# Kernel optimization log

Hardware: AMD Instinct MI355X
Metric: run time of the kernel (lower is better)

## Reference

```python
import jax, jax.numpy as jnp
import numpy as np

B, S, H = 128, 256, 768


def setup_inputs() -> dict:
    key = jax.random.key(0)
    ks = jax.random.split(key, 8)
    sc = 0.02
    return {
        "p": jax.random.normal(ks[0], (B, S, H), dtype=jnp.float32),
        "option_len": jax.random.randint(ks[1], (B,), 0, S - 1, dtype=jnp.int32),
        # SingleMatchNet params
        "Wt": jax.random.normal(ks[2], (H, H), dtype=jnp.float32) * sc,
        "bt": jnp.zeros((H,), dtype=jnp.float32),
        "Wd": jax.random.normal(ks[3], (H, H), dtype=jnp.float32) * sc,
        "bd": jnp.zeros((H,), dtype=jnp.float32),
        # AOI.dense3
        "Wd3": jax.random.normal(ks[4], (H, 3 * H), dtype=jnp.float32) * sc,
        "bd3": jnp.zeros((H,), dtype=jnp.float32),
        # FuseNet params
        "W1": jax.random.normal(ks[5], (H, H), dtype=jnp.float32) * sc,
        "b1": jnp.zeros((H,), dtype=jnp.float32),
        "W2": jax.random.normal(ks[6], (H, H), dtype=jnp.float32) * sc,
        "b2": jnp.zeros((H,), dtype=jnp.float32),
    }


def reference(p, option_len, Wt, bt, Wd, bd, Wd3, bd3, W1, b1, W2, b2):
    b, s, h = p.shape
    # For each option i, the 3 other options of its 4-option group, ascending
    others_tab = jnp.array([[1, 2, 3], [0, 2, 3], [0, 1, 3], [0, 1, 2]])
    idx = jnp.arange(b)
    others = (idx // 4)[:, None] * 4 + others_tab[idx % 4]  # [B,3]

    q = p[others]                         # [B,3,S,H] comparison options
    lens = option_len[others] + 1         # [B,3] key lengths (as in torch code)

    trans_q = q @ Wt.T + bt               # [B,3,S,H]
    att = jnp.einsum('bsh,bkth->bkst', p, trans_q)  # [B,3,S,S]

    # masked_softmax: softmax(scores*mask), zero masked, renormalize (+1e-13)
    mask = (jnp.arange(s)[None, None, None, :] < lens[:, :, None, None]).astype(p.dtype)
    sm = jax.nn.softmax(att * mask, axis=-1) * mask
    sm = sm / (sm.sum(axis=-1, keepdims=True) + 1e-13)

    att_vec = jnp.einsum('bkst,bkth->bksh', sm, q)      # [B,3,S,H]
    oc_k = jax.nn.relu(att_vec @ Wd.T + bd)             # [B,3,S,H]

    # cat along feature dim in k-order (oc1,oc2,oc3) -> [B,S,3H]
    cat_oc = oc_k.transpose(0, 2, 1, 3).reshape(b, s, 3 * h)
    oc = cat_oc @ Wd3.T + bd3                           # [B,S,H]

    # FuseNet([op, oc]): mid = sigmoid(linear1(oc) + linear2(op))
    mid = jax.nn.sigmoid(oc @ W1.T + b1 + p @ W2.T + b2)
    return p * mid + oc * (1 - mid)
```

## Files before the change

### kernel.cpp

```cpp
#include <hip/hip_runtime.h>
#include <hip/hip_bf16.h>

constexpr int Sq = 256;
constexpr int Hq = 768;
constexpr int EW = Hq * Hq;

typedef __attribute__((ext_vector_type(4))) float f32x4;
typedef __attribute__((ext_vector_type(8))) short bf16x8;

__device__ __forceinline__ float bf2f(unsigned short u) {
  unsigned int x = ((unsigned int)u) << 16;
  float f;
  __builtin_memcpy(&f, &x, 4);
  return f;
}
__device__ __forceinline__ unsigned short f2bf(float f) {
  unsigned int x;
  __builtin_memcpy(&x, &f, 4);
  unsigned int lsb = (x >> 16) & 1u;
  x += 0x7fffu + lsb;
  return (unsigned short)(x >> 16);
}
__device__ __forceinline__ ushort4 cvt4(float4 v) {
  ushort4 o;
  o.x = f2bf(v.x);
  o.y = f2bf(v.y);
  o.z = f2bf(v.z);
  o.w = f2bf(v.w);
  return o;
}
__device__ __forceinline__ void cvt4split(float4 v, ushort4& h, ushort4& l) {
  h.x = f2bf(v.x);
  l.x = f2bf(v.x - bf2f(h.x));
  h.y = f2bf(v.y);
  l.y = f2bf(v.y - bf2f(h.y));
  h.z = f2bf(v.z);
  l.z = f2bf(v.z - bf2f(h.z));
  h.w = f2bf(v.w);
  l.w = f2bf(v.w - bf2f(h.w));
}

__device__ __forceinline__ int other_of(int b, int k) {
  int i = b & 3;
  int jl = k + (k >= i ? 1 : 0);
  return (b & ~3) + jl;
}

constexpr int LDP = 32;

__device__ __forceinline__ int swz8(int row) { return ((row >> 1) & 3) << 3; }

__device__ __forceinline__ void gload16(const unsigned short* g, unsigned short* s) {
  __builtin_amdgcn_global_load_lds((const __attribute__((address_space(1))) unsigned int*)g,
                                   (__attribute__((address_space(3))) unsigned int*)s, 16, 0, 0);
}

template <int ROWS>
__device__ __forceinline__ void dma_b16(const unsigned short* __restrict__ G, int lda, int kk,
                                        unsigned short* __restrict__ S, int tid) {
#pragma unroll
  for (int pp = 0; pp < ROWS / 64; ++pp) {
    int idx = tid + pp * 256;
    int row = idx >> 2;
    int c8 = ((idx & 3) << 3) ^ swz8(row);
    gload16(G + (long)row * lda + kk + c8, S + idx * 8);
  }
}

template <int ROWS>
__device__ __forceinline__ void stage_f32(const float* __restrict__ G, int lda, int kk,
                                          unsigned short* __restrict__ S, int tid) {
#pragma unroll
  for (int pp = 0; pp < ROWS / 32; ++pp) {
    int idx = tid + pp * 256;
    int row = idx >> 3;
    int c4 = (idx & 7) << 2;
    float4 v = *(const float4*)(G + (long)row * lda + kk + c4);
    *(ushort4*)(&S[row * LDP + (c4 ^ swz8(row))]) = cvt4(v);
  }
}

template <int ROWS>
__device__ __forceinline__ void stage_f32_split(const float* __restrict__ G, int lda, int kk,
                                                unsigned short* __restrict__ Sh,
                                                unsigned short* __restrict__ Sl, int tid) {
#pragma unroll
  for (int pp = 0; pp < ROWS / 32; ++pp) {
    int idx = tid + pp * 256;
    int row = idx >> 3;
    int c4 = (idx & 7) << 2;
    float4 v = *(const float4*)(G + (long)row * lda + kk + c4);
    ushort4 h, l;
    cvt4split(v, h, l);
    int cs = c4 ^ swz8(row);
    *(ushort4*)(&Sh[row * LDP + cs]) = h;
    *(ushort4*)(&Sl[row * LDP + cs]) = l;
  }
}

__global__ __launch_bounds__(256) void k_prep_p(const float* __restrict__ p,
                                                unsigned short* __restrict__ ph,
                                                unsigned short* __restrict__ pl) {
  const long n4 = (long)128 * Sq * Hq / 4;
  const long stride = (long)gridDim.x * blockDim.x;
  for (long i = (long)blockIdx.x * blockDim.x + threadIdx.x; i < n4; i += stride) {
    float4 v = ((const float4*)p)[i];
    ushort4 h, l;
    cvt4split(v, h, l);
    ((ushort4*)ph)[i] = h;
    ((ushort4*)pl)[i] = l;
  }
}

__global__ __launch_bounds__(256) void k_prep_w(const float* __restrict__ Wt,
                                                const float* __restrict__ Wd,
                                                const float* __restrict__ Wd3,
                                                const float* __restrict__ W1,
                                                const float* __restrict__ W2,
                                                unsigned short* __restrict__ wb) {
  const int NW4 = EW / 4;
  const int stride = gridDim.x * blockDim.x;
  ushort4* Wth = (ushort4*)(wb);
  ushort4* Wtl = (ushort4*)(wb + EW);
  ushort4* Wdb = (ushort4*)(wb + 2 * EW);
  ushort4* W1b = (ushort4*)(wb + 3 * EW);
  ushort4* W2b = (ushort4*)(wb + 4 * EW);
  ushort4* Wd3b = (ushort4*)(wb + 5 * EW);
  for (int i = blockIdx.x * blockDim.x + threadIdx.x; i < NW4; i += stride) {
    float4 v = ((const float4*)Wt)[i];
    ushort4 h, l;
    cvt4split(v, h, l);
    Wth[i] = h;
    Wtl[i] = l;
    Wdb[i] = cvt4(((const float4*)Wd)[i]);
    W1b[i] = cvt4(((const float4*)W1)[i]);
    W2b[i] = cvt4(((const float4*)W2)[i]);
  }
  for (int i = blockIdx.x * blockDim.x + threadIdx.x; i < 3 * NW4; i += stride)
    Wd3b[i] = cvt4(((const float4*)Wd3)[i]);
}

template <bool A_F32, bool B_F32>
__device__ __forceinline__ void gemm_tile(const void* __restrict__ Av, int lda,
                                          const void* __restrict__ Bv, int ldb, int K,
                                          f32x4 acc[4][4]) {
  __shared__ __align__(16) unsigned short As[128 * LDP];
  __shared__ __align__(16) unsigned short Bs[128 * LDP];
  const int tid = threadIdx.x;
  const int lane = tid & 63;
  const int wid = tid >> 6;
  const int wr = (wid >> 1) << 6;
  const int wc = (wid & 1) << 6;
  const int q4 = lane >> 4;
  const int l16 = lane & 15;

#pragma unroll
  for (int mi = 0; mi < 4; ++mi)
#pragma unroll
    for (int ni = 0; ni < 4; ++ni) acc[mi][ni] = (f32x4){0.f, 0.f, 0.f, 0.f};

  for (int kk = 0; kk < K; kk += 32) {
    __syncthreads();
    if constexpr (A_F32)
      stage_f32<128>((const float*)Av, lda, kk, As, tid);
    else
      dma_b16<128>((const unsigned short*)Av, lda, kk, As, tid);
    if constexpr (B_F32)
      stage_f32<128>((const float*)Bv, ldb, kk, Bs, tid);
    else
      dma_b16<128>((const unsigned short*)Bv, ldb, kk, Bs, tid);
    __syncthreads();
    bf16x8 af[4], bfr[4];
#pragma unroll
    for (int mi = 0; mi < 4; ++mi) {
      int rr = wr + mi * 16 + l16;
      af[mi] = *(const bf16x8*)(&As[rr * LDP + ((q4 << 3) ^ swz8(rr))]);
    }
#pragma unroll
    for (int ni = 0; ni < 4; ++ni) {
      int rr = wc + ni * 16 + l16;
      bfr[ni] = *(const bf16x8*)(&Bs[rr * LDP + ((q4 << 3) ^ swz8(rr))]);
    }
#pragma unroll
    for (int mi = 0; mi < 4; ++mi)
#pragma unroll
      for (int ni = 0; ni < 4; ++ni)
        acc[mi][ni] =
            __builtin_amdgcn_mfma_f32_16x16x32_bf16(af[mi], bfr[ni], acc[mi][ni], 0, 0, 0);
  }
}

__device__ __forceinline__ void gemm_tile_split(const unsigned short* __restrict__ Ahp,
                                                const unsigned short* __restrict__ Alp, int lda,
                                                const float* __restrict__ B, int ldb, int K,
                                                f32x4 acc[4][4]) {
  __shared__ __align__(16) unsigned short Ah[128 * LDP], Al[128 * LDP];
  __shared__ __align__(16) unsigned short Bh[128 * LDP], Bl[128 * LDP];
  const int tid = threadIdx.x;
  const int lane = tid & 63;
  const int wid = tid >> 6;
  const int wr = (wid >> 1) << 6;
  const int wc = (wid & 1) << 6;
  const int q4 = lane >> 4;
  const int l16 = lane & 15;

#pragma unroll
  for (int mi = 0; mi < 4; ++mi)
#pragma unroll
    for (int ni = 0; ni < 4; ++ni) acc[mi][ni] = (f32x4){0.f, 0.f, 0.f, 0.f};

  for (int kk = 0; kk < K; kk += 32) {
    __syncthreads();
    dma_b16<128>(Ahp, lda, kk, Ah, tid);
    dma_b16<128>(Alp, lda, kk, Al, tid);
    stage_f32_split<128>(B, ldb, kk, Bh, Bl, tid);
    __syncthreads();
    bf16x8 ah[4], al[4], bh[4], bl[4];
#pragma unroll
    for (int mi = 0; mi < 4; ++mi) {
      int rr = wr + mi * 16 + l16;
      int co = (q4 << 3) ^ swz8(rr);
      ah[mi] = *(const bf16x8*)(&Ah[rr * LDP + co]);
      al[mi] = *(const bf16x8*)(&Al[rr * LDP + co]);
    }
#pragma unroll
    for (int ni = 0; ni < 4; ++ni) {
      int rr = wc + ni * 16 + l16;
      int co = (q4 << 3) ^ swz8(rr);
      bh[ni] = *(const bf16x8*)(&Bh[rr * LDP + co]);
      bl[ni] = *(const bf16x8*)(&Bl[rr * LDP + co]);
    }
#pragma unroll
    for (int mi = 0; mi < 4; ++mi)
#pragma unroll
      for (int ni = 0; ni < 4; ++ni) {
        acc[mi][ni] =
            __builtin_amdgcn_mfma_f32_16x16x32_bf16(ah[mi], bh[ni], acc[mi][ni], 0, 0, 0);
        acc[mi][ni] =
            __builtin_amdgcn_mfma_f32_16x16x32_bf16(ah[mi], bl[ni], acc[mi][ni], 0, 0, 0);
        acc[mi][ni] =
            __builtin_amdgcn_mfma_f32_16x16x32_bf16(al[mi], bh[ni], acc[mi][ni], 0, 0, 0);
      }
  }
}

__device__ __forceinline__ void gemm_tile_split_b16(const unsigned short* __restrict__ Ahp,
                                                    const unsigned short* __restrict__ Alp, int lda,
                                                    const unsigned short* __restrict__ Bhp,
                                                    const unsigned short* __restrict__ Blp, int ldb,
                                                    int K, f32x4 acc[4][4]) {
  __shared__ __align__(16) unsigned short Ah[128 * LDP], Al[128 * LDP];
  __shared__ __align__(16) unsigned short Bh[128 * LDP], Bl[128 * LDP];
  const int tid = threadIdx.x;
  const int lane = tid & 63;
  const int wid = tid >> 6;
  const int wr = (wid >> 1) << 6;
  const int wc = (wid & 1) << 6;
  const int q4 = lane >> 4;
  const int l16 = lane & 15;

#pragma unroll
  for (int mi = 0; mi < 4; ++mi)
#pragma unroll
    for (int ni = 0; ni < 4; ++ni) acc[mi][ni] = (f32x4){0.f, 0.f, 0.f, 0.f};

  for (int kk = 0; kk < K; kk += 32) {
    __syncthreads();
    dma_b16<128>(Ahp, lda, kk, Ah, tid);
    dma_b16<128>(Alp, lda, kk, Al, tid);
    dma_b16<128>(Bhp, ldb, kk, Bh, tid);
    dma_b16<128>(Blp, ldb, kk, Bl, tid);
    __syncthreads();
    bf16x8 ah[4], al[4], bh[4], bl[4];
#pragma unroll
    for (int mi = 0; mi < 4; ++mi) {
      int rr = wr + mi * 16 + l16;
      int co = (q4 << 3) ^ swz8(rr);
      ah[mi] = *(const bf16x8*)(&Ah[rr * LDP + co]);
      al[mi] = *(const bf16x8*)(&Al[rr * LDP + co]);
    }
#pragma unroll
    for (int ni = 0; ni < 4; ++ni) {
      int rr = wc + ni * 16 + l16;
      int co = (q4 << 3) ^ swz8(rr);
      bh[ni] = *(const bf16x8*)(&Bh[rr * LDP + co]);
      bl[ni] = *(const bf16x8*)(&Bl[rr * LDP + co]);
    }
#pragma unroll
    for (int mi = 0; mi < 4; ++mi)
#pragma unroll
      for (int ni = 0; ni < 4; ++ni) {
        acc[mi][ni] =
            __builtin_amdgcn_mfma_f32_16x16x32_bf16(ah[mi], bh[ni], acc[mi][ni], 0, 0, 0);
        acc[mi][ni] =
            __builtin_amdgcn_mfma_f32_16x16x32_bf16(ah[mi], bl[ni], acc[mi][ni], 0, 0, 0);
        acc[mi][ni] =
            __builtin_amdgcn_mfma_f32_16x16x32_bf16(al[mi], bh[ni], acc[mi][ni], 0, 0, 0);
      }
  }
}

#define EPI_BEGIN()                                        \
  const int lane = threadIdx.x & 63;                       \
  const int wid = threadIdx.x >> 6;                        \
  const int wr = (wid >> 1) << 6, wc = (wid & 1) << 6;     \
  const int q4 = lane >> 4, l16 = lane & 15;               \
  _Pragma("unroll") for (int mi = 0; mi < 4; ++mi)         \
      _Pragma("unroll") for (int ni = 0; ni < 4; ++ni)

template <bool WF32>
__global__ __launch_bounds__(256) void k_tp(const unsigned short* __restrict__ ph,
                                            const unsigned short* __restrict__ pl,
                                            const void* __restrict__ Wh,
                                            const void* __restrict__ Wl,
                                            const float* __restrict__ bt,
                                            unsigned short* __restrict__ tph,
                                            unsigned short* __restrict__ tpl) {
  const int bm = blockIdx.x * 128, bn = blockIdx.y * 128;
  f32x4 acc[4][4];
  if constexpr (WF32)
    gemm_tile_split(ph + (long)bm * Hq, pl + (long)bm * Hq, Hq,
                    (const float*)Wh + (long)bn * Hq, Hq, Hq, acc);
  else
    gemm_tile_split_b16(ph + (long)bm * Hq, pl + (long)bm * Hq, Hq,
                        (const unsigned short*)Wh + (long)bn * Hq,
                        (const unsigned short*)Wl + (long)bn * Hq, Hq, Hq, acc);
  const bool has_lo = (tpl != nullptr);
  EPI_BEGIN() {
    int col = bn + wc + ni * 16 + l16;
    float bv = bt[col];
#pragma unroll
    for (int r = 0; r < 4; ++r) {
      int row = bm + wr + mi * 16 + q4 * 4 + r;
      float v = acc[mi][ni][r] + bv;
      unsigned short h = f2bf(v);
      tph[(long)row * Hq + col] = h;
      if (has_lo) tpl[(long)row * Hq + col] = f2bf(v - bf2f(h));
    }
  }
}

template <bool WF32>
__global__ __launch_bounds__(256) void k_pd(const unsigned short* __restrict__ ph,
                                            const void* __restrict__ Wd,
                                            unsigned short* __restrict__ pdT) {
  const int bm = blockIdx.x * 128, bn = blockIdx.y * 128;
  f32x4 acc[4][4];
  if constexpr (WF32)
    gemm_tile<false, true>(ph + (long)bm * Hq, Hq, (const float*)Wd + (long)bn * Hq, Hq, Hq, acc);
  else
    gemm_tile<false, false>(ph + (long)bm * Hq, Hq, (const unsigned short*)Wd + (long)bn * Hq,
                            Hq, Hq, acc);
  EPI_BEGIN() {
    int col = bn + wc + ni * 16 + l16;
    int rbase = bm + wr + mi * 16 + (q4 << 2);
    int b = rbase >> 8, s0 = rbase & 255;
    ushort4 o;
    o.x = f2bf(acc[mi][ni][0]);
    o.y = f2bf(acc[mi][ni][1]);
    o.z = f2bf(acc[mi][ni][2]);
    o.w = f2bf(acc[mi][ni][3]);
    *(ushort4*)(pdT + ((long)b * Hq + col) * Sq + s0) = o;
  }
}

__global__ __launch_bounds__(256, 1) void k_attsm(const unsigned short* __restrict__ ph,
                                                  const unsigned short* __restrict__ pl,
                                                  const unsigned short* __restrict__ tph,
                                                  const unsigned short* __restrict__ tpl,
                                                  const int* __restrict__ olen,
                                                  unsigned short* __restrict__ sm) {
  const int lin = blockIdx.x + 2 * blockIdx.y;
  const int w = (lin & 7) * 96 + (lin >> 3);
  const int batch = w >> 1;
  const int bm = (w & 1) * 128;

  const int b = batch / 3, k = batch % 3;
  const int j = other_of(b, k);
  const int len = olen[j] + 1;
  const int tid = threadIdx.x;
  const int lane = tid & 63;
  const int wid = tid >> 6;
  const int wr = (wid >> 1) << 6;
  const int wc = (wid & 1) << 7;
  const int half = wid & 1;
  const int q4 = lane >> 4, l16 = lane & 15;
  const bool has_lo = (tpl != nullptr);

  __shared__ __align__(16) unsigned short Ah[128 * LDP], Al[128 * LDP];
  __shared__ __align__(16) unsigned short Bh[256 * LDP], Bl[256 * LDP];
  __shared__ float red[256];

  const unsigned short* Aph = ph + ((long)b * Sq + bm) * Hq;
  const unsigned short* Apl = pl + ((long)b * Sq + bm) * Hq;
  const unsigned short* Bph = tph + (long)j * Sq * Hq;
  const unsigned short* Bpl = has_lo ? tpl + (long)j * Sq * Hq : nullptr;

  f32x4 acc[4][8];
#pragma unroll
  for (int mi = 0; mi < 4; ++mi)
#pragma unroll
    for (int ni = 0; ni < 8; ++ni) acc[mi][ni] = (f32x4){0.f, 0.f, 0.f, 0.f};

  for (int kk = 0; kk < Hq; kk += 32) {
    __syncthreads();
    dma_b16<128>(Aph, Hq, kk, Ah, tid);
    dma_b16<128>(Apl, Hq, kk, Al, tid);
    dma_b16<256>(Bph, Hq, kk, Bh, tid);
    if (has_lo) dma_b16<256>(Bpl, Hq, kk, Bl, tid);
    __syncthreads();
    bf16x8 ah[4], al[4];
#pragma unroll
    for (int mi = 0; mi < 4; ++mi) {
      int rr = wr + mi * 16 + l16;
      int co = (q4 << 3) ^ swz8(rr);
      ah[mi] = *(const bf16x8*)(&Ah[rr * LDP + co]);
      al[mi] = *(const bf16x8*)(&Al[rr * LDP + co]);
    }
#pragma unroll
    for (int ni = 0; ni < 8; ++ni) {
      int rr = wc + ni * 16 + l16;
      int co = (q4 << 3) ^ swz8(rr);
      bf16x8 bh = *(const bf16x8*)(&Bh[rr * LDP + co]);
#pragma unroll
      for (int mi = 0; mi < 4; ++mi) {
        acc[mi][ni] = __builtin_amdgcn_mfma_f32_16x16x32_bf16(ah[mi], bh, acc[mi][ni], 0, 0, 0);
        acc[mi][ni] = __builtin_amdgcn_mfma_f32_16x16x32_bf16(al[mi], bh, acc[mi][ni], 0, 0, 0);
      }
      if (has_lo) {
        bf16x8 bl = *(const bf16x8*)(&Bl[rr * LDP + co]);
#pragma unroll
        for (int mi = 0; mi < 4; ++mi)
          acc[mi][ni] = __builtin_amdgcn_mfma_f32_16x16x32_bf16(ah[mi], bl, acc[mi][ni], 0, 0, 0);
      }
    }
  }

  bool cm[8];
#pragma unroll
  for (int ni = 0; ni < 8; ++ni) cm[ni] = (wc + ni * 16 + l16) >= len;
#pragma unroll
  for (int mi = 0; mi < 4; ++mi)
#pragma unroll
    for (int ni = 0; ni < 8; ++ni)
      if (cm[ni]) acc[mi][ni] = (f32x4){0.f, 0.f, 0.f, 0.f};

  float rmax[4][4];
#pragma unroll
  for (int mi = 0; mi < 4; ++mi)
#pragma unroll
    for (int r = 0; r < 4; ++r) {
      float m = acc[mi][0][r];
#pragma unroll
      for (int ni = 1; ni < 8; ++ni) m = fmaxf(m, acc[mi][ni][r]);
#pragma unroll
      for (int off = 1; off <= 8; off <<= 1) m = fmaxf(m, __shfl_xor(m, off, 64));
      rmax[mi][r] = m;
    }
  if (l16 == 0) {
#pragma unroll
    for (int mi = 0; mi < 4; ++mi)
#pragma unroll
      for (int r = 0; r < 4; ++r) red[(wr + mi * 16 + q4 * 4 + r) * 2 + half] = rmax[mi][r];
  }
  __syncthreads();
#pragma unroll
  for (int mi = 0; mi < 4; ++mi)
#pragma unroll
    for (int r = 0; r < 4; ++r) {
      int row = wr + mi * 16 + q4 * 4 + r;
      rmax[mi][r] = fmaxf(red[row * 2], red[row * 2 + 1]);
    }
  __syncthreads();

  float rsum[4][4];
#pragma unroll
  for (int mi = 0; mi < 4; ++mi)
#pragma unroll
    for (int r = 0; r < 4; ++r) rsum[mi][r] = 0.f;
#pragma unroll
  for (int mi = 0; mi < 4; ++mi)
#pragma unroll
    for (int ni = 0; ni < 8; ++ni)
#pragma unroll
      for (int r = 0; r < 4; ++r) {
        float e = __expf(acc[mi][ni][r] - rmax[mi][r]);
        acc[mi][ni][r] = e;
        if (!cm[ni]) rsum[mi][r] += e;
      }
#pragma unroll
  for (int mi = 0; mi < 4; ++mi)
#pragma unroll
    for (int r = 0; r < 4; ++r) {
#pragma unroll
      for (int off = 1; off <= 8; off <<= 1) rsum[mi][r] += __shfl_xor(rsum[mi][r], off, 64);
    }
  if (l16 == 0) {
#pragma unroll
    for (int mi = 0; mi < 4; ++mi)
#pragma unroll
      for (int r = 0; r < 4; ++r) red[(wr + mi * 16 + q4 * 4 + r) * 2 + half] = rsum[mi][r];
  }
  __syncthreads();

  const float nm = (float)(Sq - len);
  unsigned short* srow = sm + (long)batch * Sq * Sq;
#pragma unroll
  for (int mi = 0; mi < 4; ++mi)
#pragma unroll
    for (int r = 0; r < 4; ++r) {
      int row = wr + mi * 16 + q4 * 4 + r;
      float su = red[row * 2] + red[row * 2 + 1];
      float em = __expf(-rmax[mi][r]);
      float zs = su + nm * em;
      float fs = 1.f / (su + 1e-13f * zs);
      unsigned short* o = srow + (long)(bm + row) * Sq + wc + l16;
#pragma unroll
      for (int ni = 0; ni < 8; ++ni)
        o[ni * 16] = f2bf(cm[ni] ? 0.f : acc[mi][ni][r] * fs);
    }
}

__global__ __launch_bounds__(256) void k_occ(const unsigned short* __restrict__ sm,
                                             const unsigned short* __restrict__ pdT,
                                             const float* __restrict__ bd,
                                             unsigned short* __restrict__ occ) {
  const int lin = blockIdx.x + 2 * (blockIdx.y + 6 * blockIdx.z);
  const int w = (lin & 7) * 576 + (lin >> 3);
  const int t = w >> 1;
  const int bm = (w & 1) * 128, bn = (t % 6) * 128;
  const int batch = t / 6;

  const int b = batch / 3, k = batch % 3;
  const int j = other_of(b, k);
  f32x4 acc[4][4];
  gemm_tile<false, false>(sm + (long)batch * Sq * Sq + (long)bm * Sq, Sq,
                          pdT + ((long)j * Hq + bn) * Sq, Sq, Sq, acc);
  EPI_BEGIN() {
    int col = bn + wc + ni * 16 + l16;
    float bv = bd[col];
#pragma unroll
    for (int r = 0; r < 4; ++r) {
      int s = bm + wr + mi * 16 + q4 * 4 + r;
      occ[((long)(b * Sq + s) * 3 + k) * Hq + col] = f2bf(fmaxf(acc[mi][ni][r] + bv, 0.f));
    }
  }
}

template <bool WF32>
__global__ __launch_bounds__(256) void k_oc(const unsigned short* __restrict__ occ,
                                            const void* __restrict__ Wd3,
                                            const float* __restrict__ bd3,
                                            unsigned short* __restrict__ oc) {
  const int bm = blockIdx.x * 128, bn = blockIdx.y * 128;
  f32x4 acc[4][4];
  if constexpr (WF32)
    gemm_tile<false, true>(occ + (long)bm * 3 * Hq, 3 * Hq,
                           (const float*)Wd3 + (long)bn * 3 * Hq, 3 * Hq, 3 * Hq, acc);
  else
    gemm_tile<false, false>(occ + (long)bm * 3 * Hq, 3 * Hq,
                            (const unsigned short*)Wd3 + (long)bn * 3 * Hq, 3 * Hq, 3 * Hq, acc);
  EPI_BEGIN() {
    int col = bn + wc + ni * 16 + l16;
    float bv = bd3[col];
#pragma unroll
    for (int r = 0; r < 4; ++r) {
      int row = bm + wr + mi * 16 + q4 * 4 + r;
      oc[(long)row * Hq + col] = f2bf(acc[mi][ni][r] + bv);
    }
  }
}

template <bool WF32>
__global__ __launch_bounds__(256) void k_g1(const unsigned short* __restrict__ oc,
                                            const void* __restrict__ W1,
                                            const float* __restrict__ b1,
                                            const float* __restrict__ b2,
                                            unsigned short* __restrict__ g1) {
  const int bm = blockIdx.x * 128, bn = blockIdx.y * 128;
  f32x4 acc[4][4];
  if constexpr (WF32)
    gemm_tile<false, true>(oc + (long)bm * Hq, Hq, (const float*)W1 + (long)bn * Hq, Hq, Hq, acc);
  else
    gemm_tile<false, false>(oc + (long)bm * Hq, Hq, (const unsigned short*)W1 + (long)bn * Hq,
                            Hq, Hq, acc);
  EPI_BEGIN() {
    int col = bn + wc + ni * 16 + l16;
    float bv = b1[col] + b2[col];
#pragma unroll
    for (int r = 0; r < 4; ++r) {
      int row = bm + wr + mi * 16 + q4 * 4 + r;
      g1[(long)row * Hq + col] = f2bf(acc[mi][ni][r] + bv);
    }
  }
}

template <bool WF32>
__global__ __launch_bounds__(256) void k_out(const float* __restrict__ p,
                                             const void* __restrict__ W2,
                                             const unsigned short* __restrict__ g1,
                                             const unsigned short* __restrict__ oc,
                                             float* __restrict__ out) {
  const int bm = blockIdx.x * 128, bn = blockIdx.y * 128;
  f32x4 acc[4][4];
  if constexpr (WF32)
    gemm_tile<true, true>(p + (long)bm * Hq, Hq, (const float*)W2 + (long)bn * Hq, Hq, Hq, acc);
  else
    gemm_tile<true, false>(p + (long)bm * Hq, Hq, (const unsigned short*)W2 + (long)bn * Hq,
                           Hq, Hq, acc);
  EPI_BEGIN() {
    int col = bn + wc + ni * 16 + l16;
#pragma unroll
    for (int r = 0; r < 4; ++r) {
      int row = bm + wr + mi * 16 + q4 * 4 + r;
      long idx = (long)row * Hq + col;
      float g = acc[mi][ni][r] + bf2f(g1[idx]);
      float mid = 1.f / (1.f + __expf(-g));
      float pv = p[idx];
      float ov = bf2f(oc[idx]);
      out[idx] = pv * mid + ov * (1.f - mid);
    }
  }
}

extern "C" void kernel_launch(void* const* d_in, const int* in_sizes, int n_in, void* d_out,
                              int out_size, void* d_ws, size_t ws_size, hipStream_t stream) {
  const float* p = (const float*)d_in[0];
  const int* olen = (const int*)d_in[1];
  const float* Wt = (const float*)d_in[2];
  const float* bt = (const float*)d_in[3];
  const float* Wd = (const float*)d_in[4];
  const float* bd = (const float*)d_in[5];
  const float* Wd3 = (const float*)d_in[6];
  const float* bd3 = (const float*)d_in[7];
  const float* W1 = (const float*)d_in[8];
  const float* b1 = (const float*)d_in[9];
  const float* W2 = (const float*)d_in[10];
  const float* b2 = (const float*)d_in[11];
  float* out = (float*)d_out;

  char* ws = (char*)d_ws;
  const long U = 50331648L;
  const long WB = 9437184L;

  if (ws_size >= (size_t)(WB + 5 * U)) {
    unsigned short* wb = (unsigned short*)(ws);
    unsigned short* ph = (unsigned short*)(ws + WB);
    unsigned short* pl = (unsigned short*)(ws + WB + 1 * U);
    unsigned short* tph = (unsigned short*)(ws + WB + 2 * U);
    unsigned short* tpl = (unsigned short*)(ws + WB + 3 * U);
    unsigned short* sm = (unsigned short*)(ws + WB + 4 * U);
    unsigned short* pdT = (unsigned short*)(ws + WB + 3 * U);
    unsigned short* occ = (unsigned short*)(ws + WB);
    unsigned short* oc = (unsigned short*)(ws + WB + 3 * U);
    unsigned short* g1 = (unsigned short*)(ws + WB + 4 * U);

    k_prep_p<<<2048, 256, 0, stream>>>(p, ph, pl);
    k_prep_w<<<512, 256, 0, stream>>>(Wt, Wd, Wd3, W1, W2, wb);
    k_tp<false><<<dim3(256, 6), 256, 0, stream>>>(ph, pl, wb, wb + EW, bt, tph, tpl);
    k_attsm<<<dim3(2, 384), 256, 0, stream>>>(ph, pl, tph, tpl, olen, sm);
    k_pd<false><<<dim3(256, 6), 256, 0, stream>>>(ph, wb + 2 * EW, pdT);
    k_occ<<<dim3(2, 6, 384), 256, 0, stream>>>(sm, pdT, bd, occ);
    k_oc<false><<<dim3(256, 6), 256, 0, stream>>>(occ, wb + 5 * EW, bd3, oc);
    k_g1<false><<<dim3(256, 6), 256, 0, stream>>>(oc, wb + 3 * EW, b1, b2, g1);
    k_out<false><<<dim3(256, 6), 256, 0, stream>>>(p, wb + 4 * EW, g1, oc, out);
  } else {
    unsigned short* tph = (unsigned short*)(ws + 0 * U);
    unsigned short* tpl = nullptr;
    unsigned short* ph = (unsigned short*)(ws + 1 * U);
    unsigned short* pl = (unsigned short*)(ws + 2 * U);
    unsigned short* occ = (unsigned short*)(ws + 0 * U);
    unsigned short* pdT = (unsigned short*)(ws + 3 * U);
    unsigned short* oc = (unsigned short*)(ws + 3 * U);
    unsigned short* sm = (unsigned short*)(ws + 4 * U);
    unsigned short* g1 = (unsigned short*)(ws + 4 * U);

    k_prep_p<<<2048, 256, 0, stream>>>(p, ph, pl);
    k_tp<true><<<dim3(256, 6), 256, 0, stream>>>(ph, pl, Wt, nullptr, bt, tph, tpl);
    k_pd<true><<<dim3(256, 6), 256, 0, stream>>>(ph, Wd, pdT);
    k_attsm<<<dim3(2, 384), 256, 0, stream>>>(ph, pl, tph, tpl, olen, sm);
    k_occ<<<dim3(2, 6, 384), 256, 0, stream>>>(sm, pdT, bd, occ);
    k_oc<true><<<dim3(256, 6), 256, 0, stream>>>(occ, Wd3, bd3, oc);
    k_g1<true><<<dim3(256, 6), 256, 0, stream>>>(oc, W1, b1, b2, g1);
    k_out<true><<<dim3(256, 6), 256, 0, stream>>>(p, W2, g1, oc, out);
  }
}
```

Baseline: 966.5 us.

## Double-buffer LDS tiles in GEMMs and load attention A operand directly from global

Converts the shared GEMM tile loops and the attention-score kernel to double-buffered LDS staging. The next K-slice is staged while MFMAs run on the current one, which removes one barrier per iteration. In the attention kernel the A operand (p hi/lo) is now read straight from global memory into registers instead of being staged in LDS, and launch bounds are raised to allow two blocks per CU. This roughly doubles B-tile LDS use and adds uncoalesced global A loads in exchange for more overlap and occupancy. An extra barrier is added before the reduction buffer is reused.

New measurement: 938.1 us (median of 2 runs). 1.03x faster.

```diff
diff --git a/kernel.cpp b/kernel.cpp
--- a/kernel.cpp
+++ b/kernel.cpp
@@ -144,8 +144,8 @@
 __device__ __forceinline__ void gemm_tile(const void* __restrict__ Av, int lda,
                                           const void* __restrict__ Bv, int ldb, int K,
                                           f32x4 acc[4][4]) {
-  __shared__ __align__(16) unsigned short As[128 * LDP];
-  __shared__ __align__(16) unsigned short Bs[128 * LDP];
+  __shared__ __align__(16) unsigned short As[2][128 * LDP];
+  __shared__ __align__(16) unsigned short Bs[2][128 * LDP];
   const int tid = threadIdx.x;
   const int lane = tid & 63;
   const int wid = tid >> 6;
@@ -159,34 +159,49 @@
 #pragma unroll
     for (int ni = 0; ni < 4; ++ni) acc[mi][ni] = (f32x4){0.f, 0.f, 0.f, 0.f};
 
-  for (int kk = 0; kk < K; kk += 32) {
-    __syncthreads();
+  auto STAGE = [&](int kk, int bi) {
     if constexpr (A_F32)
-      stage_f32<128>((const float*)Av, lda, kk, As, tid);
+      stage_f32<128>((const float*)Av, lda, kk, As[bi], tid);
     else
-      dma_b16<128>((const unsigned short*)Av, lda, kk, As, tid);
+      dma_b16<128>((const unsigned short*)Av, lda, kk, As[bi], tid);
     if constexpr (B_F32)
-      stage_f32<128>((const float*)Bv, ldb, kk, Bs, tid);
+      stage_f32<128>((const float*)Bv, ldb, kk, Bs[bi], tid);
     else
-      dma_b16<128>((const unsigned short*)Bv, ldb, kk, Bs, tid);
-    __syncthreads();
-    bf16x8 af[4], bfr[4];
+      dma_b16<128>((const unsigned short*)Bv, ldb, kk, Bs[bi], tid);
+  };
+  bf16x8 af[4], bfr[4];
+  auto READF = [&](int bi) {
 #pragma unroll
     for (int mi = 0; mi < 4; ++mi) {
       int rr = wr + mi * 16 + l16;
-      af[mi] = *(const bf16x8*)(&As[rr * LDP + ((q4 << 3) ^ swz8(rr))]);
+      af[mi] = *(const bf16x8*)(&As[bi][rr * LDP + ((q4 << 3) ^ swz8(rr))]);
     }
 #pragma unroll
     for (int ni = 0; ni < 4; ++ni) {
       int rr = wc + ni * 16 + l16;
-      bfr[ni] = *(const bf16x8*)(&Bs[rr * LDP + ((q4 << 3) ^ swz8(rr))]);
-    }
+      bfr[ni] = *(const bf16x8*)(&Bs[bi][rr * LDP + ((q4 << 3) ^ swz8(rr))]);
+    }
+  };
+  auto DOMFMA = [&]() {
 #pragma unroll
     for (int mi = 0; mi < 4; ++mi)
 #pragma unroll
       for (int ni = 0; ni < 4; ++ni)
         acc[mi][ni] =
             __builtin_amdgcn_mfma_f32_16x16x32_bf16(af[mi], bfr[ni], acc[mi][ni], 0, 0, 0);
+  };
+
+  const int ns = K >> 5;
+  STAGE(0, 0);
+  for (int i = 0; i < ns; i += 2) {
+    __syncthreads();
+    READF(0);
+    STAGE((i + 1) << 5, 1);
+    DOMFMA();
+    __syncthreads();
+    READF(1);
+    if (i + 2 < ns) STAGE((i + 2) << 5, 0);
+    DOMFMA();
   }
 }
 
@@ -249,8 +264,8 @@
                                                     const unsigned short* __restrict__ Bhp,
                                                     const unsigned short* __restrict__ Blp, int ldb,
                                                     int K, f32x4 acc[4][4]) {
-  __shared__ __align__(16) unsigned short Ah[128 * LDP], Al[128 * LDP];
-  __shared__ __align__(16) unsigned short Bh[128 * LDP], Bl[128 * LDP];
+  __shared__ __align__(16) unsigned short Ah[2][128 * LDP], Al[2][128 * LDP];
+  __shared__ __align__(16) unsigned short Bh[2][128 * LDP], Bl[2][128 * LDP];
   const int tid = threadIdx.x;
   const int lane = tid & 63;
   const int wid = tid >> 6;
@@ -264,28 +279,30 @@
 #pragma unroll
     for (int ni = 0; ni < 4; ++ni) acc[mi][ni] = (f32x4){0.f, 0.f, 0.f, 0.f};
 
-  for (int kk = 0; kk < K; kk += 32) {
-    __syncthreads();
-    dma_b16<128>(Ahp, lda, kk, Ah, tid);
-    dma_b16<128>(Alp, lda, kk, Al, tid);
-    dma_b16<128>(Bhp, ldb, kk, Bh, tid);
-    dma_b16<128>(Blp, ldb, kk, Bl, tid);
-    __syncthreads();
-    bf16x8 ah[4], al[4], bh[4], bl[4];
+  auto STAGE = [&](int kk, int bi) {
+    dma_b16<128>(Ahp, lda, kk, Ah[bi], tid);
+    dma_b16<128>(Alp, lda, kk, Al[bi], tid);
+    dma_b16<128>(Bhp, ldb, kk, Bh[bi], tid);
+    dma_b16<128>(Blp, ldb, kk, Bl[bi], tid);
+  };
+  bf16x8 ah[4], al[4], bh[4], bl[4];
+  auto READF = [&](int bi) {
 #pragma unroll
     for (int mi = 0; mi < 4; ++mi) {
       int rr = wr + mi * 16 + l16;
       int co = (q4 << 3) ^ swz8(rr);
-      ah[mi] = *(const bf16x8*)(&Ah[rr * LDP + co]);
-      al[mi] = *(const bf16x8*)(&Al[rr * LDP + co]);
+      ah[mi] = *(const bf16x8*)(&Ah[bi][rr * LDP + co]);
+      al[mi] = *(const bf16x8*)(&Al[bi][rr * LDP + co]);
     }
 #pragma unroll
     for (int ni = 0; ni < 4; ++ni) {
       int rr = wc + ni * 16 + l16;
       int co = (q4 << 3) ^ swz8(rr);
-      bh[ni] = *(const bf16x8*)(&Bh[rr * LDP + co]);
-      bl[ni] = *(const bf16x8*)(&Bl[rr * LDP + co]);
-    }
+      bh[ni] = *(const bf16x8*)(&Bh[bi][rr * LDP + co]);
+      bl[ni] = *(const bf16x8*)(&Bl[bi][rr * LDP + co]);
+    }
+  };
+  auto DOMFMA = [&]() {
 #pragma unroll
     for (int mi = 0; mi < 4; ++mi)
 #pragma unroll
@@ -297,6 +314,19 @@
         acc[mi][ni] =
             __builtin_amdgcn_mfma_f32_16x16x32_bf16(al[mi], bh[ni], acc[mi][ni], 0, 0, 0);
       }
+  };
+
+  const int ns = K >> 5;
+  STAGE(0, 0);
+  for (int i = 0; i < ns; i += 2) {
+    __syncthreads();
+    READF(0);
+    STAGE((i + 1) << 5, 1);
+    DOMFMA();
+    __syncthreads();
+    READF(1);
+    if (i + 2 < ns) STAGE((i + 2) << 5, 0);
+    DOMFMA();
   }
 }
 
@@ -364,7 +394,7 @@
   }
 }
 
-__global__ __launch_bounds__(256, 1) void k_attsm(const unsigned short* __restrict__ ph,
+__global__ __launch_bounds__(256, 2) void k_attsm(const unsigned short* __restrict__ ph,
                                                   const unsigned short* __restrict__ pl,
                                                   const unsigned short* __restrict__ tph,
                                                   const unsigned short* __restrict__ tpl,
@@ -387,8 +417,7 @@
   const int q4 = lane >> 4, l16 = lane & 15;
   const bool has_lo = (tpl != nullptr);
 
-  __shared__ __align__(16) unsigned short Ah[128 * LDP], Al[128 * LDP];
-  __shared__ __align__(16) unsigned short Bh[256 * LDP], Bl[256 * LDP];
+  __shared__ __align__(16) unsigned short Bh[2][256 * LDP], Bl[2][256 * LDP];
   __shared__ float red[256];
 
   const unsigned short* Aph = ph + ((long)b * Sq + bm) * Hq;
@@ -402,38 +431,50 @@
 #pragma unroll
     for (int ni = 0; ni < 8; ++ni) acc[mi][ni] = (f32x4){0.f, 0.f, 0.f, 0.f};
 
-  for (int kk = 0; kk < Hq; kk += 32) {
-    __syncthreads();
-    dma_b16<128>(Aph, Hq, kk, Ah, tid);
-    dma_b16<128>(Apl, Hq, kk, Al, tid);
-    dma_b16<256>(Bph, Hq, kk, Bh, tid);
-    if (has_lo) dma_b16<256>(Bpl, Hq, kk, Bl, tid);
-    __syncthreads();
-    bf16x8 ah[4], al[4];
+  auto STAGE_B = [&](int kk, int bi) {
+    dma_b16<256>(Bph, Hq, kk, Bh[bi], tid);
+    if (has_lo) dma_b16<256>(Bpl, Hq, kk, Bl[bi], tid);
+  };
+  bf16x8 ah[4], al[4];
+  auto LOADA = [&](int kk) {
 #pragma unroll
     for (int mi = 0; mi < 4; ++mi) {
-      int rr = wr + mi * 16 + l16;
-      int co = (q4 << 3) ^ swz8(rr);
-      ah[mi] = *(const bf16x8*)(&Ah[rr * LDP + co]);
-      al[mi] = *(const bf16x8*)(&Al[rr * LDP + co]);
-    }
+      long off = (long)(wr + mi * 16 + l16) * Hq + kk + (q4 << 3);
+      ah[mi] = *(const bf16x8*)(Aph + off);
+      al[mi] = *(const bf16x8*)(Apl + off);
+    }
+  };
+  auto COMPUTE = [&](int bi) {
 #pragma unroll
     for (int ni = 0; ni < 8; ++ni) {
       int rr = wc + ni * 16 + l16;
       int co = (q4 << 3) ^ swz8(rr);
-      bf16x8 bh = *(const bf16x8*)(&Bh[rr * LDP + co]);
+      bf16x8 bh = *(const bf16x8*)(&Bh[bi][rr * LDP + co]);
 #pragma unroll
       for (int mi = 0; mi < 4; ++mi) {
         acc[mi][ni] = __builtin_amdgcn_mfma_f32_16x16x32_bf16(ah[mi], bh, acc[mi][ni], 0, 0, 0);
         acc[mi][ni] = __builtin_amdgcn_mfma_f32_16x16x32_bf16(al[mi], bh, acc[mi][ni], 0, 0, 0);
       }
       if (has_lo) {
-        bf16x8 bl = *(const bf16x8*)(&Bl[rr * LDP + co]);
+        bf16x8 bl = *(const bf16x8*)(&Bl[bi][rr * LDP + co]);
 #pragma unroll
         for (int mi = 0; mi < 4; ++mi)
           acc[mi][ni] = __builtin_amdgcn_mfma_f32_16x16x32_bf16(ah[mi], bl, acc[mi][ni], 0, 0, 0);
       }
     }
+  };
+
+  const int ns = Hq / 32;
+  STAGE_B(0, 0);
+  for (int i = 0; i < ns; i += 2) {
+    __syncthreads();
+    LOADA(i << 5);
+    STAGE_B((i + 1) << 5, 1);
+    COMPUTE(0);
+    __syncthreads();
+    LOADA((i + 1) << 5);
+    if (i + 2 < ns) STAGE_B((i + 2) << 5, 0);
+    COMPUTE(1);
   }
 
   bool cm[8];
@@ -457,6 +498,7 @@
       for (int off = 1; off <= 8; off <<= 1) m = fmaxf(m, __shfl_xor(m, off, 64));
       rmax[mi][r] = m;
     }
+  __syncthreads();
   if (l16 == 0) {
 #pragma unroll
     for (int mi = 0; mi < 4; ++mi)
```
